# Kernel tuning notes

Measured on AMD Instinct MI355X. Metric: run time of the kernel, lower is better.

The kernel has to match this reference:

```python
import jax, jax.numpy as jnp
import numpy as np

N = 100000
E = 3200000
F_IN = 128


def gcn_conv(x, w, b, src, dst, n):
    """PyG GCNConv: out = D^-1/2 (A + I) D^-1/2 (x @ w) + b.
    src/dst already include self loops."""
    xw = x @ w                                   # [N, F_out]
    ones = jnp.ones(src.shape[0], dtype=xw.dtype)
    deg = jax.ops.segment_sum(ones, dst, num_segments=n)   # in-degree incl. self loop
    dinv = jnp.where(deg > 0, jax.lax.rsqrt(deg), 0.0)
    norm = dinv[src] * dinv[dst]                 # [E+N]
    msg = xw[src] * norm[:, None]                # gather + scale
    out = jax.ops.segment_sum(msg, dst, num_segments=n)
    return out + b


def setup_inputs() -> dict:
    key = jax.random.key(0)
    ks = jax.random.split(key, 10)
    x = jax.random.normal(ks[0], (N, F_IN), dtype=jnp.float32)
    edge_index = jax.random.randint(ks[1], (2, E), 0, N, dtype=jnp.int64)
    # Glorot-ish init for weights
    def lin(k, fi, fo):
        return jax.random.normal(k, (fi, fo), dtype=jnp.float32) / np.sqrt(fi)
    return {
        "x": x,
        "edge_index": edge_index,
        "w1": lin(ks[2], F_IN, 64), "b1": jnp.zeros((64,), jnp.float32),
        "w2": lin(ks[3], 64, 32),   "b2": jnp.zeros((32,), jnp.float32),
        "w3": lin(ks[4], 32, 16),   "b3": jnp.zeros((16,), jnp.float32),
        "w_out": lin(ks[5], 16, 1), "b_out": jnp.zeros((1,), jnp.float32),
    }


def reference(x, edge_index, w1, b1, w2, b2, w3, b3, w_out, b_out):
    n = x.shape[0]
    # add self loops once (PyG adds them inside each GCNConv; same graph => same result)
    loop = jnp.arange(n, dtype=edge_index.dtype)
    src = jnp.concatenate([edge_index[0], loop])
    dst = jnp.concatenate([edge_index[1], loop])
    h = jax.nn.relu(gcn_conv(x, w1, b1, src, dst, n))
    h = jax.nn.relu(gcn_conv(h, w2, b2, src, dst, n))
    h = jax.nn.relu(gcn_conv(h, w3, b3, src, dst, n))
    return h @ w_out + b_out  # [N, 1]
```

## Files before the change

### kernel.cpp

```cpp
#include <hip/hip_runtime.h>
#include <hip/hip_bf16.h>


#define NBUCK 391
#define BSHIFT 8
#define CAP 10240
#define EPB 2048

typedef __attribute__((ext_vector_type(2))) unsigned short ushort2v;
typedef __attribute__((ext_vector_type(4))) unsigned short ushort4v;
typedef __attribute__((ext_vector_type(8))) unsigned short ushort8v;
typedef __attribute__((ext_vector_type(8))) _Float16 half8;
typedef __attribute__((ext_vector_type(4))) float f32x4;

__device__ __forceinline__ float bf2f(unsigned short u) {
  union { unsigned int i; float f; } v;
  v.i = ((unsigned int)u) << 16;
  return v.f;
}
__device__ __forceinline__ unsigned short f2bf(float f) {
  union { float f; unsigned int i; } v;
  v.f = f;
  unsigned int r = v.i + 0x7FFF + ((v.i >> 16) & 1);
  return (unsigned short)(r >> 16);
}

static __global__ __launch_bounds__(256) void partition_kernel(
    const int* __restrict__ src, const int* __restrict__ dst,
    int* __restrict__ bucket_cnt, int* __restrict__ part, int E) {
  __shared__ int hist[NBUCK];
  __shared__ int bbase[NBUCK];
  const int t = threadIdx.x;
  for (int j = t; j < NBUCK; j += 256) hist[j] = 0;
  __syncthreads();
  const int base = blockIdx.x * EPB + t * 8;
  int ss[8], dd[8];
  if (base + 8 <= E) {
    int4 s0 = *(const int4*)&src[base], s1 = *(const int4*)&src[base + 4];
    int4 d0 = *(const int4*)&dst[base], d1 = *(const int4*)&dst[base + 4];
    ss[0] = s0.x; ss[1] = s0.y; ss[2] = s0.z; ss[3] = s0.w;
    ss[4] = s1.x; ss[5] = s1.y; ss[6] = s1.z; ss[7] = s1.w;
    dd[0] = d0.x; dd[1] = d0.y; dd[2] = d0.z; dd[3] = d0.w;
    dd[4] = d1.x; dd[5] = d1.y; dd[6] = d1.z; dd[7] = d1.w;
  } else {
#pragma unroll
    for (int j = 0; j < 8; ++j) {
      int i = base + j;
      ss[j] = (i < E) ? src[i] : -1;
      dd[j] = (i < E) ? dst[i] : 0;
    }
  }
#pragma unroll
  for (int j = 0; j < 8; ++j)
    if (ss[j] >= 0) atomicAdd(&hist[dd[j] >> BSHIFT], 1);
  __syncthreads();
  for (int j = t; j < NBUCK; j += 256) {
    int h = hist[j];
    bbase[j] = h ? atomicAdd(&bucket_cnt[j], h) : 0;
    hist[j] = 0;
  }
  __syncthreads();
#pragma unroll
  for (int j = 0; j < 8; ++j) {
    if (ss[j] >= 0) {
      int b = dd[j] >> BSHIFT;
      int r = bbase[b] + atomicAdd(&hist[b], 1);
      if (r < CAP) part[(size_t)b * CAP + r] = ((dd[j] & 255) << 17) | ss[j];
    }
  }
}

static __global__ __launch_bounds__(256) void bucket2csr_kernel(
    const int* __restrict__ bucket_cnt, const int* __restrict__ part,
    int* __restrict__ csr_src, int* __restrict__ row_start,
    int* __restrict__ row_end, float* __restrict__ dinv, int n) {
  __shared__ int plds[CAP];
  __shared__ int hist[256];
  __shared__ int cursor[256];
  __shared__ int sdata[256];
  const int b = blockIdx.x;
  const int t = threadIdx.x;
  const int base = b * CAP;
  int cnt = bucket_cnt[b];
  if (cnt > CAP) cnt = CAP;
  hist[t] = 0;
  __syncthreads();
  int i = t * 4;
  for (; i + 4 <= cnt; i += 1024) {
    int4 v = *(const int4*)&part[base + i];
    *(int4*)&plds[i] = v;
    atomicAdd(&hist[v.x >> 17], 1);
    atomicAdd(&hist[v.y >> 17], 1);
    atomicAdd(&hist[v.z >> 17], 1);
    atomicAdd(&hist[v.w >> 17], 1);
  }
  for (int k = i; k < cnt && k < i + 4; ++k) {
    int pv = part[base + k];
    plds[k] = pv;
    atomicAdd(&hist[pv >> 17], 1);
  }
  __syncthreads();
  const int v = hist[t];
  const int pd = (v + 7) & ~7;
  sdata[t] = pd;
  __syncthreads();
  int incl = pd;
  for (int off = 1; off < 256; off <<= 1) {
    int y = (t >= off) ? sdata[t - off] : 0;
    __syncthreads();
    incl += y;
    sdata[t] = incl;
    __syncthreads();
  }
  const int excl = incl - pd;
  cursor[t] = excl;
  const int node = b * 256 + t;
  if (node < n) {
    row_start[node] = base + excl;
    row_end[node] = base + excl + pd;
    dinv[node] = rsqrtf((float)(v + 1));
  }
  __syncthreads();
  for (int k = t; k < cnt; k += 256) {
    int pv = plds[k];
    int pos = atomicAdd(&cursor[pv >> 17], 1);
    csr_src[base + pos] = pv & 0x1FFFF;
  }
  for (int k = v; k < pd; ++k) csr_src[base + excl + k] = n;
}

static __global__ __launch_bounds__(256) void gemm1_mfma_kernel(
    const float* __restrict__ x, const float* __restrict__ w1,
    const float* __restrict__ dinv, unsigned short* __restrict__ xws, int n) {
  __shared__ _Float16 xa[64 * 128];
  __shared__ _Float16 wt[64 * 128];
  const int t = threadIdx.x;
  const int base = blockIdx.x * 64;
  for (int i = t; i < 64 * 16; i += 256) {
    int r = i >> 4, k8 = i & 15;
    int node = base + r;
    float4 a = {0.f, 0.f, 0.f, 0.f}, b = {0.f, 0.f, 0.f, 0.f};
    if (node < n) {
      a = *(const float4*)&x[(size_t)node * 128 + k8 * 8];
      b = *(const float4*)&x[(size_t)node * 128 + k8 * 8 + 4];
    }
    half8 h = {(_Float16)a.x, (_Float16)a.y, (_Float16)a.z, (_Float16)a.w,
               (_Float16)b.x, (_Float16)b.y, (_Float16)b.z, (_Float16)b.w};
    int byte = (r * 256 + k8 * 16) ^ ((r & 7) << 4);
    *(half8*)((char*)xa + byte) = h;
  }
  for (int i = t; i < 128 * 64; i += 256) {
    int k = i >> 6, o = i & 63;
    _Float16 v = (_Float16)w1[i];
    int byte = (o * 256 + k * 2) ^ ((o & 7) << 4);
    *(_Float16*)((char*)wt + byte) = v;
  }
  __syncthreads();
  const int wv = t >> 6;
  const int lane = t & 63;
  const int m = lane & 15;
  const int kg = lane >> 4;
  const int arow = wv * 16 + m;
  f32x4 acc[4] = {{0.f, 0.f, 0.f, 0.f}, {0.f, 0.f, 0.f, 0.f},
                  {0.f, 0.f, 0.f, 0.f}, {0.f, 0.f, 0.f, 0.f}};
#pragma unroll
  for (int ks = 0; ks < 4; ++ks) {
    int k0 = ks * 32 + kg * 8;
    int abyte = (arow * 256 + k0 * 2) ^ ((arow & 7) << 4);
    half8 af = *(const half8*)((const char*)xa + abyte);
#pragma unroll
    for (int nt = 0; nt < 4; ++nt) {
      int o = nt * 16 + m;
      int bbyte = (o * 256 + k0 * 2) ^ ((o & 7) << 4);
      half8 bf = *(const half8*)((const char*)wt + bbyte);
      acc[nt] = __builtin_amdgcn_mfma_f32_16x16x32_f16(af, bf, acc[nt], 0, 0, 0);
    }
  }
#pragma unroll
  for (int r = 0; r < 4; ++r) {
    int node = base + wv * 16 + kg * 4 + r;
    if (node < n) {
      float dv = dinv[node];
#pragma unroll
      for (int nt = 0; nt < 4; ++nt)
        xws[(size_t)node * 64 + nt * 16 + m] = f2bf(dv * acc[nt][r]);
    }
  }
}

template <int F, int FOUT>
static __global__ __launch_bounds__(256) void agg_gemm_kernel(
    const unsigned short* __restrict__ xws, const int* __restrict__ row_start,
    const int* __restrict__ row_end, const int* __restrict__ csr_src,
    const float* __restrict__ dinv, const float* __restrict__ bias,
    const float* __restrict__ W, unsigned short* __restrict__ xws_next, int n) {
  constexpr int GC = F / 8;
  constexpr int LPN = F / 4;
  constexpr int NODES = 256 / LPN;
  constexpr int OUTS = FOUT / LPN;
  __shared__ float ws[F * FOUT];
  __shared__ float hs[NODES][F + 1];
  const int t = threadIdx.x;
  for (int i = t; i < F * FOUT / 4; i += 256)
    *(float4*)&ws[i * 4] = *(const float4*)&W[i * 4];
  const int nl = t / LPN;
  const int l = t % LPN;
  const int c = l % GC;
  const int sub = l / GC;
  const int node = blockIdx.x * NODES + nl;
  const bool valid = node < n;
  const int safe = valid ? node : 0;
  const int start = valid ? row_start[safe] : 0;
  const int end = valid ? row_end[safe] : 0;
  float acc[8] = {0.f, 0.f, 0.f, 0.f, 0.f, 0.f, 0.f, 0.f};
  for (int e = start + sub * 8; e < end; e += 16) {
    int4 sa = *(const int4*)&csr_src[e];
    int4 sb = *(const int4*)&csr_src[e + 4];
    ushort8v v0 = *(const ushort8v*)&xws[(size_t)sa.x * F + c * 8];
    ushort8v v1 = *(const ushort8v*)&xws[(size_t)sa.y * F + c * 8];
    ushort8v v2 = *(const ushort8v*)&xws[(size_t)sa.z * F + c * 8];
    ushort8v v3 = *(const ushort8v*)&xws[(size_t)sa.w * F + c * 8];
    ushort8v v4 = *(const ushort8v*)&xws[(size_t)sb.x * F + c * 8];
    ushort8v v5 = *(const ushort8v*)&xws[(size_t)sb.y * F + c * 8];
    ushort8v v6 = *(const ushort8v*)&xws[(size_t)sb.z * F + c * 8];
    ushort8v v7 = *(const ushort8v*)&xws[(size_t)sb.w * F + c * 8];
#pragma unroll
    for (int j = 0; j < 8; ++j)
      acc[j] += ((bf2f(v0[j]) + bf2f(v1[j])) + (bf2f(v2[j]) + bf2f(v3[j]))) +
                ((bf2f(v4[j]) + bf2f(v5[j])) + (bf2f(v6[j]) + bf2f(v7[j])));
  }
#pragma unroll
  for (int j = 0; j < 8; ++j) acc[j] += __shfl_xor(acc[j], GC);
  const float dv = dinv[safe];
  if (sub == 0) {
    ushort8v sv = *(const ushort8v*)&xws[(size_t)safe * F + c * 8];
#pragma unroll
    for (int j = 0; j < 8; ++j)
      hs[nl][c * 8 + j] =
          fmaxf(dv * (acc[j] + bf2f(sv[j])) + bias[c * 8 + j], 0.f);
  }
  __syncthreads();
  float o[OUTS];
#pragma unroll
  for (int j = 0; j < OUTS; ++j) o[j] = 0.f;
#pragma unroll 4
  for (int k = 0; k < F; ++k) {
    float hv = hs[nl][k];
#pragma unroll
    for (int j = 0; j < OUTS; ++j) o[j] += hv * ws[k * FOUT + l * OUTS + j];
  }
  if (valid) {
    ushort2v r = {f2bf(dv * o[0]), f2bf(dv * o[1])};
    *(ushort2v*)&xws_next[(size_t)node * FOUT + l * OUTS] = r;
  }
}

static __global__ __launch_bounds__(256) void agg_head_kernel(
    const unsigned short* __restrict__ xws, const int* __restrict__ row_start,
    const int* __restrict__ row_end, const int* __restrict__ csr_src,
    const float* __restrict__ dinv, const float* __restrict__ bias,
    float* __restrict__ out, const float* __restrict__ w_out,
    const float* __restrict__ b_out, int n) {
  constexpr int F = 16, NODES = 64;
  const int t = threadIdx.x;
  const int nl = t >> 2;
  const int l = t & 3;
  const int c = l & 1;
  const int sub = l >> 1;
  const int node = blockIdx.x * NODES + nl;
  if (node >= n) return;
  const int start = row_start[node], end = row_end[node];
  float acc[8] = {0.f, 0.f, 0.f, 0.f, 0.f, 0.f, 0.f, 0.f};
  for (int e = start + sub * 8; e < end; e += 16) {
    int4 sa = *(const int4*)&csr_src[e];
    int4 sb = *(const int4*)&csr_src[e + 4];
    ushort8v v0 = *(const ushort8v*)&xws[(size_t)sa.x * F + c * 8];
    ushort8v v1 = *(const ushort8v*)&xws[(size_t)sa.y * F + c * 8];
    ushort8v v2 = *(const ushort8v*)&xws[(size_t)sa.z * F + c * 8];
    ushort8v v3 = *(const ushort8v*)&xws[(size_t)sa.w * F + c * 8];
    ushort8v v4 = *(const ushort8v*)&xws[(size_t)sb.x * F + c * 8];
    ushort8v v5 = *(const ushort8v*)&xws[(size_t)sb.y * F + c * 8];
    ushort8v v6 = *(const ushort8v*)&xws[(size_t)sb.z * F + c * 8];
    ushort8v v7 = *(const ushort8v*)&xws[(size_t)sb.w * F + c * 8];
#pragma unroll
    for (int j = 0; j < 8; ++j)
      acc[j] += ((bf2f(v0[j]) + bf2f(v1[j])) + (bf2f(v2[j]) + bf2f(v3[j]))) +
                ((bf2f(v4[j]) + bf2f(v5[j])) + (bf2f(v6[j]) + bf2f(v7[j])));
  }
#pragma unroll
  for (int j = 0; j < 8; ++j) acc[j] += __shfl_xor(acc[j], 2);
  ushort8v sv = *(const ushort8v*)&xws[(size_t)node * F + c * 8];
  float dv = dinv[node];
  float p = 0.f;
#pragma unroll
  for (int j = 0; j < 8; ++j) {
    float r = fmaxf(dv * (acc[j] + bf2f(sv[j])) + bias[c * 8 + j], 0.f);
    p += r * w_out[c * 8 + j];
  }
  p += __shfl_xor(p, 1);
  if (l == 0) out[node] = p + b_out[0];
}

extern "C" void kernel_launch(void* const* d_in, const int* in_sizes, int n_in,
                              void* d_out, int out_size, void* d_ws, size_t ws_size,
                              hipStream_t stream) {
  const float* x     = (const float*)d_in[0];
  const int*   ei    = (const int*)d_in[1];
  const float* w1    = (const float*)d_in[2];
  const float* b1    = (const float*)d_in[3];
  const float* w2    = (const float*)d_in[4];
  const float* b2    = (const float*)d_in[5];
  const float* w3    = (const float*)d_in[6];
  const float* b3    = (const float*)d_in[7];
  const float* w_out = (const float*)d_in[8];
  const float* b_out = (const float*)d_in[9];
  float* out = (float*)d_out;

  const int n = in_sizes[0] / 128;
  const int E = in_sizes[1] / 2;
  const int* srcA = ei;
  const int* dstA = ei + E;

  char* p = (char*)d_ws;
  auto carve = [&](size_t bytes) {
    void* r = (void*)p;
    p += (bytes + 255) & ~(size_t)255;
    return r;
  };
  const size_t partBytes = (size_t)NBUCK * CAP * 4;
  int*   csr_src    = (int*)carve(partBytes);
  int*   bucket_cnt = (int*)carve((size_t)NBUCK * 4);
  int*   row_start  = (int*)carve((size_t)n * 4);
  int*   row_end    = (int*)carve((size_t)n * 4);
  float* dinv       = (float*)carve((size_t)n * 4);
  char*  regionP    = (char*)carve(partBytes);
  int*   part       = (int*)regionP;
  unsigned short* xws1 = (unsigned short*)regionP;
  unsigned short* xws2 = (unsigned short*)carve((size_t)(n + 1) * 32 * 2);
  unsigned short* xws3 = (unsigned short*)carve((size_t)(n + 1) * 16 * 2);

  hipMemsetAsync(bucket_cnt, 0, (size_t)NBUCK * 4, stream);
  partition_kernel<<<(E + EPB - 1) / EPB, 256, 0, stream>>>(srcA, dstA,
                                                            bucket_cnt, part, E);
  bucket2csr_kernel<<<NBUCK, 256, 0, stream>>>(bucket_cnt, part, csr_src,
                                               row_start, row_end, dinv, n);
  hipMemsetAsync(xws1 + (size_t)n * 64, 0, 64 * 2, stream);
  hipMemsetAsync(xws2 + (size_t)n * 32, 0, 32 * 2, stream);
  hipMemsetAsync(xws3 + (size_t)n * 16, 0, 16 * 2, stream);

  gemm1_mfma_kernel<<<(n + 63) / 64, 256, 0, stream>>>(x, w1, dinv, xws1, n);
  agg_gemm_kernel<64, 32><<<(n + 15) / 16, 256, 0, stream>>>(
      xws1, row_start, row_end, csr_src, dinv, b1, w2, xws2, n);
  agg_gemm_kernel<32, 16><<<(n + 31) / 32, 256, 0, stream>>>(
      xws2, row_start, row_end, csr_src, dinv, b2, w3, xws3, n);
  agg_head_kernel<<<(n + 63) / 64, 256, 0, stream>>>(
      xws3, row_start, row_end, csr_src, dinv, b3, out, w_out, b_out, n);
}
```

Before: 215.5 us.

## Locally sort edge tiles in LDS before bucket scatter and stage CSR output

The partition kernel now processes 4096-edge tiles. It builds a per-tile bucket histogram, scans it, and sorts the packed edges into shared memory. It then copies each bucket's contiguous run to global memory, instead of scattering every edge with its own global write. bucket2csr now builds the per-node ordering in shared memory and writes csr_src with coalesced int4 stores, re-reading part from global memory instead of caching it. Costs: dst is read twice, there are extra scans and barriers, and the final per-bucket copy is serial per thread.

```diff
diff --git a/kernel.cpp b/kernel.cpp
--- a/kernel.cpp
+++ b/kernel.cpp
@@ -5,7 +5,7 @@
 #define NBUCK 391
 #define BSHIFT 8
 #define CAP 10240
-#define EPB 2048
+#define TILE 4096
 
 typedef __attribute__((ext_vector_type(2))) unsigned short ushort2v;
 typedef __attribute__((ext_vector_type(4))) unsigned short ushort4v;
@@ -28,45 +28,86 @@
 static __global__ __launch_bounds__(256) void partition_kernel(
     const int* __restrict__ src, const int* __restrict__ dst,
     int* __restrict__ bucket_cnt, int* __restrict__ part, int E) {
-  __shared__ int hist[NBUCK];
-  __shared__ int bbase[NBUCK];
+  __shared__ int sorted[TILE];
+  __shared__ int hist[512];
+  __shared__ int lstart[512];
+  __shared__ int cur[512];
+  __shared__ int gbase[512];
+  __shared__ int sdata[256];
   const int t = threadIdx.x;
-  for (int j = t; j < NBUCK; j += 256) hist[j] = 0;
-  __syncthreads();
-  const int base = blockIdx.x * EPB + t * 8;
-  int ss[8], dd[8];
-  if (base + 8 <= E) {
-    int4 s0 = *(const int4*)&src[base], s1 = *(const int4*)&src[base + 4];
-    int4 d0 = *(const int4*)&dst[base], d1 = *(const int4*)&dst[base + 4];
-    ss[0] = s0.x; ss[1] = s0.y; ss[2] = s0.z; ss[3] = s0.w;
-    ss[4] = s1.x; ss[5] = s1.y; ss[6] = s1.z; ss[7] = s1.w;
-    dd[0] = d0.x; dd[1] = d0.y; dd[2] = d0.z; dd[3] = d0.w;
-    dd[4] = d1.x; dd[5] = d1.y; dd[6] = d1.z; dd[7] = d1.w;
-  } else {
-#pragma unroll
-    for (int j = 0; j < 8; ++j) {
-      int i = base + j;
-      ss[j] = (i < E) ? src[i] : -1;
-      dd[j] = (i < E) ? dst[i] : 0;
+  const int base0 = blockIdx.x * TILE;
+  hist[t] = 0;
+  hist[t + 256] = 0;
+  __syncthreads();
+  for (int i = t * 4; i < TILE; i += 1024) {
+    int gi = base0 + i;
+    if (gi + 4 <= E) {
+      int4 d = *(const int4*)&dst[gi];
+      atomicAdd(&hist[d.x >> BSHIFT], 1);
+      atomicAdd(&hist[d.y >> BSHIFT], 1);
+      atomicAdd(&hist[d.z >> BSHIFT], 1);
+      atomicAdd(&hist[d.w >> BSHIFT], 1);
+    } else {
+      for (int k = 0; k < 4 && gi + k < E; ++k)
+        atomicAdd(&hist[dst[gi + k] >> BSHIFT], 1);
     }
   }
-#pragma unroll
-  for (int j = 0; j < 8; ++j)
-    if (ss[j] >= 0) atomicAdd(&hist[dd[j] >> BSHIFT], 1);
-  __syncthreads();
-  for (int j = t; j < NBUCK; j += 256) {
-    int h = hist[j];
-    bbase[j] = h ? atomicAdd(&bucket_cnt[j], h) : 0;
-    hist[j] = 0;
-  }
-  __syncthreads();
-#pragma unroll
-  for (int j = 0; j < 8; ++j) {
-    if (ss[j] >= 0) {
-      int b = dd[j] >> BSHIFT;
-      int r = bbase[b] + atomicAdd(&hist[b], 1);
-      if (r < CAP) part[(size_t)b * CAP + r] = ((dd[j] & 255) << 17) | ss[j];
+  __syncthreads();
+  const int v0 = hist[2 * t], v1 = hist[2 * t + 1];
+  const int s = v0 + v1;
+  sdata[t] = s;
+  __syncthreads();
+  int incl = s;
+  for (int off = 1; off < 256; off <<= 1) {
+    int y = (t >= off) ? sdata[t - off] : 0;
+    __syncthreads();
+    incl += y;
+    sdata[t] = incl;
+    __syncthreads();
+  }
+  const int excl = incl - s;
+  lstart[2 * t] = excl;
+  lstart[2 * t + 1] = excl + v0;
+  cur[2 * t] = 0;
+  cur[2 * t + 1] = 0;
+  if (2 * t < NBUCK && v0) gbase[2 * t] = atomicAdd(&bucket_cnt[2 * t], v0);
+  if (2 * t + 1 < NBUCK && v1)
+    gbase[2 * t + 1] = atomicAdd(&bucket_cnt[2 * t + 1], v1);
+  __syncthreads();
+  for (int i = t * 4; i < TILE; i += 1024) {
+    int gi = base0 + i;
+    if (gi + 4 <= E) {
+      int4 d = *(const int4*)&dst[gi];
+      int4 sc = *(const int4*)&src[gi];
+      int b0 = d.x >> BSHIFT, b1 = d.y >> BSHIFT;
+      int b2 = d.z >> BSHIFT, b3 = d.w >> BSHIFT;
+      int p0 = lstart[b0] + atomicAdd(&cur[b0], 1);
+      sorted[p0] = ((d.x & 255) << 17) | sc.x;
+      int p1 = lstart[b1] + atomicAdd(&cur[b1], 1);
+      sorted[p1] = ((d.y & 255) << 17) | sc.y;
+      int p2 = lstart[b2] + atomicAdd(&cur[b2], 1);
+      sorted[p2] = ((d.z & 255) << 17) | sc.z;
+      int p3 = lstart[b3] + atomicAdd(&cur[b3], 1);
+      sorted[p3] = ((d.w & 255) << 17) | sc.w;
+    } else {
+      for (int k = 0; k < 4 && gi + k < E; ++k) {
+        int d = dst[gi + k], sc = src[gi + k];
+        int b = d >> BSHIFT;
+        int pos = lstart[b] + atomicAdd(&cur[b], 1);
+        sorted[pos] = ((d & 255) << 17) | sc;
+      }
     }
+  }
+  __syncthreads();
+  for (int b = t; b < NBUCK; b += 256) {
+    int h = hist[b];
+    if (!h) continue;
+    int gb = gbase[b];
+    int lim = CAP - gb;
+    if (lim > h) lim = h;
+    const int ls = lstart[b];
+    int* dstp = &part[(size_t)b * CAP + gb];
+    for (int k = 0; k < lim; ++k) dstp[k] = sorted[ls + k];
   }
 }
 
@@ -74,7 +115,7 @@
     const int* __restrict__ bucket_cnt, const int* __restrict__ part,
     int* __restrict__ csr_src, int* __restrict__ row_start,
     int* __restrict__ row_end, float* __restrict__ dinv, int n) {
-  __shared__ int plds[CAP];
+  __shared__ int sorted[CAP];
   __shared__ int hist[256];
   __shared__ int cursor[256];
   __shared__ int sdata[256];
@@ -88,17 +129,13 @@
   int i = t * 4;
   for (; i + 4 <= cnt; i += 1024) {
     int4 v = *(const int4*)&part[base + i];
-    *(int4*)&plds[i] = v;
     atomicAdd(&hist[v.x >> 17], 1);
     atomicAdd(&hist[v.y >> 17], 1);
     atomicAdd(&hist[v.z >> 17], 1);
     atomicAdd(&hist[v.w >> 17], 1);
   }
-  for (int k = i; k < cnt && k < i + 4; ++k) {
-    int pv = part[base + k];
-    plds[k] = pv;
-    atomicAdd(&hist[pv >> 17], 1);
-  }
+  for (int k = i; k < cnt && k < i + 4; ++k)
+    atomicAdd(&hist[part[base + k] >> 17], 1);
   __syncthreads();
   const int v = hist[t];
   const int pd = (v + 7) & ~7;
@@ -113,6 +150,7 @@
     __syncthreads();
   }
   const int excl = incl - pd;
+  const int ptot = sdata[255];
   cursor[t] = excl;
   const int node = b * 256 + t;
   if (node < n) {
@@ -121,12 +159,27 @@
     dinv[node] = rsqrtf((float)(v + 1));
   }
   __syncthreads();
-  for (int k = t; k < cnt; k += 256) {
-    int pv = plds[k];
+  i = t * 4;
+  for (; i + 4 <= cnt; i += 1024) {
+    int4 pv = *(const int4*)&part[base + i];
+    int p0 = atomicAdd(&cursor[pv.x >> 17], 1);
+    sorted[p0] = pv.x & 0x1FFFF;
+    int p1 = atomicAdd(&cursor[pv.y >> 17], 1);
+    sorted[p1] = pv.y & 0x1FFFF;
+    int p2 = atomicAdd(&cursor[pv.z >> 17], 1);
+    sorted[p2] = pv.z & 0x1FFFF;
+    int p3 = atomicAdd(&cursor[pv.w >> 17], 1);
+    sorted[p3] = pv.w & 0x1FFFF;
+  }
+  for (int k = i; k < cnt && k < i + 4; ++k) {
+    int pv = part[base + k];
     int pos = atomicAdd(&cursor[pv >> 17], 1);
-    csr_src[base + pos] = pv & 0x1FFFF;
-  }
-  for (int k = v; k < pd; ++k) csr_src[base + excl + k] = n;
+    sorted[pos] = pv & 0x1FFFF;
+  }
+  for (int k = v; k < pd; ++k) sorted[excl + k] = n;
+  __syncthreads();
+  for (int j = t * 4; j + 4 <= ptot; j += 1024)
+    *(int4*)&csr_src[base + j] = *(const int4*)&sorted[j];
 }
 
 static __global__ __launch_bounds__(256) void gemm1_mfma_kernel(
@@ -340,8 +393,8 @@
   unsigned short* xws3 = (unsigned short*)carve((size_t)(n + 1) * 16 * 2);
 
   hipMemsetAsync(bucket_cnt, 0, (size_t)NBUCK * 4, stream);
-  partition_kernel<<<(E + EPB - 1) / EPB, 256, 0, stream>>>(srcA, dstA,
-                                                            bucket_cnt, part, E);
+  partition_kernel<<<(E + TILE - 1) / TILE, 256, 0, stream>>>(srcA, dstA,
+                                                              bucket_cnt, part, E);
   bucket2csr_kernel<<<NBUCK, 256, 0, stream>>>(bucket_cnt, part, csr_src,
                                                row_start, row_end, dinv, n);
   hipMemsetAsync(xws1 + (size_t)n * 64, 0, 64 * 2, stream);
```

Measured after the change: 198.1 us. -8.1%, faster.
